# Performance work log

Measured on AMD Instinct MI355X. Metric: run time of the kernel, lower is better.

## Reference

```python
import jax, jax.numpy as jnp
import numpy as np

NEG = -1e9


def setup_inputs() -> dict:
    key = jax.random.key(0)
    ks = jax.random.split(key, 10)
    B, C, H, W = 4, 64, 64, 64
    Cq = C // 8
    x = jax.random.normal(ks[0], (B, C, H, W), dtype=jnp.float32)
    mask = jax.random.randint(ks[1], (B, 1, H, W), 0, 2, dtype=jnp.int32)
    # 1x1 conv params (out_ch, in_ch) + bias
    Wq = jax.random.normal(ks[2], (Cq, C), dtype=jnp.float32) * (1.0 / np.sqrt(C))
    bq = jnp.zeros((Cq,), dtype=jnp.float32)
    Wk = jax.random.normal(ks[3], (Cq, C), dtype=jnp.float32) * (1.0 / np.sqrt(C))
    bk = jnp.zeros((Cq,), dtype=jnp.float32)
    Wv = jax.random.normal(ks[4], (C, C), dtype=jnp.float32) * (1.0 / np.sqrt(C))
    bv = jnp.zeros((C,), dtype=jnp.float32)
    # torch inits gamma to 0; use small random so attention path contributes
    gamma = jax.random.normal(ks[5], (1,), dtype=jnp.float32) * 0.1
    return {"x": x, "mask": mask, "Wq": Wq, "bq": bq, "Wk": Wk, "bk": bk,
            "Wv": Wv, "bv": bv, "gamma": gamma}


def reference(x, mask, Wq, bq, Wk, bk, Wv, bv, gamma):
    B, C, H, W = x.shape
    N = H * W
    xf = x.reshape(B, C, N)                      # (B,C,N)
    # 1x1 convs == per-pixel linear projections
    q = jnp.einsum('oc,bcn->bno', Wq, xf) + bq   # (B,N,Cq)
    k = jnp.einsum('oc,bcn->bon', Wk, xf) + bk[None, :, None]  # (B,Cq,N)
    v = jnp.einsum('oc,bcn->bon', Wv, xf) + bv[None, :, None]  # (B,C,N)
    m = mask.reshape(B, N).astype(bool)
    logits = jnp.einsum('bno,bom->bnm', q, k)    # (B,N,N)
    valid = m[:, :, None] & m[:, None, :]        # outer-product validity mask
    logits = jnp.where(valid, logits, NEG)
    attn = jax.nn.softmax(logits, axis=-1)       # (B,N,N)
    out = jnp.einsum('bcj,bij->bci', v, attn)    # (B,C,N)
    out = out.reshape(B, C, H, W)
    return gamma * out + x
```

## Files before the change

kernel.cpp:

```cpp
#include <hip/hip_runtime.h>

typedef unsigned int uint;
typedef unsigned short ushort;
typedef unsigned long long ull;
typedef __attribute__((ext_vector_type(8))) short short8;
typedef __attribute__((ext_vector_type(4))) float f32x4;
typedef __attribute__((ext_vector_type(16))) float f32x16;
typedef __attribute__((ext_vector_type(4))) uint uint4v;
typedef __attribute__((ext_vector_type(2))) uint uint2v;

#define BATCH 4
#define CH 64
#define NPIX 4096
#define LOG2E 1.44269504f

#define WSQ 0
#define WSK 262144
#define WSV 524288
#define WSNV 1572864
#define WSQM 1572928
#define WSVPU 1589312

__device__ __forceinline__ ushort f2bf(float f) {
    union { float f; uint u; } a; a.f = f;
    const uint u = a.u;
    return (ushort)((u + 0x7FFFu + ((u >> 16) & 1u)) >> 16);
}
__device__ __forceinline__ uint cvtpk(float a, float b) {
    uint r;
    asm("v_cvt_pk_bf16_f32 %0, %1, %2" : "=v"(r) : "v"(a), "v"(b));
    return r;
}

__global__ __launch_bounds__(256) void proj_kernel(
    const float* __restrict__ x, const int* __restrict__ mask,
    const float* __restrict__ Wq, const float* __restrict__ bq,
    const float* __restrict__ Wk, const float* __restrict__ bk,
    const float* __restrict__ Wv, const float* __restrict__ bv,
    ushort* __restrict__ ws)
{
    __shared__ int   wcnt[4];
    __shared__ float wvs[4][16];
    const int g = blockIdx.y;
    const int tid = threadIdx.x;
    const int wid = tid >> 6, lane = tid & 63;

    const int pix = blockIdx.x * 256 + tid;
    const int b = pix >> 12;
    const int n = pix & (NPIX - 1);
    const int qm = mask[pix];
    const ull bal = __ballot(qm != 0);
    if (lane == 0) wcnt[wid] = __popcll(bal);
    __syncthreads();

    const float* xb = x + (size_t)b * CH * NPIX + n;
    float xv[64];
#pragma unroll
    for (int c = 0; c < 64; c++) xv[c] = xb[(size_t)c * NPIX];

    float acc[16];
    if (g == 0) {
#pragma unroll
        for (int o = 0; o < 16; o++) {
            const float* Wrow = (o < 8) ? (Wq + o * 64) : (Wk + (o - 8) * 64);
            float a = (o < 8) ? bq[o] : bk[o - 8];
#pragma unroll
            for (int c4 = 0; c4 < 16; c4++) {
                const float4 w = *(const float4*)(Wrow + c4 * 4);
                a += w.x * xv[c4 * 4] + w.y * xv[c4 * 4 + 1]
                   + w.z * xv[c4 * 4 + 2] + w.w * xv[c4 * 4 + 3];
            }
            acc[o] = a;
        }
    } else {
        const float* Wg = Wv + (g - 1) * 16 * 64;
        const float* bg = bv + (g - 1) * 16;
#pragma unroll
        for (int o = 0; o < 16; o++) {
            const float* Wrow = Wg + o * 64;
            float a = bg[o];
#pragma unroll
            for (int c4 = 0; c4 < 16; c4++) {
                const float4 w = *(const float4*)(Wrow + c4 * 4);
                a += w.x * xv[c4 * 4] + w.y * xv[c4 * 4 + 1]
                   + w.z * xv[c4 * 4 + 2] + w.w * xv[c4 * 4 + 3];
            }
            acc[o] = a;
        }
    }

    int offV = 0, offI = 0, nvb = 0;
#pragma unroll
    for (int w = 0; w < 4; w++) {
        const int cw = wcnt[w];
        if (w < wid) { offV += cw; offI += 64 - cw; }
        nvb += cw;
    }
    const int rankV = __popcll(bal & ((1ull << lane) - 1ull));
    const int slot = qm ? (offV + rankV) : (nvb + offI + (lane - rankV));
    const int rr = n >> 8;
    const int js = rr * 8 + (slot >> 5);
    const int jl = slot & 31;

    if (g == 0) {
        {
            const int jtq = n >> 5, jlq = n & 31;
            const float s = qm ? LOG2E : 0.f;
            uint4v lo, hi;
            lo.x = cvtpk(acc[0] * s, acc[1] * s);
            lo.y = cvtpk(acc[2] * s, acc[3] * s);
            lo.z = cvtpk(acc[4] * s, acc[5] * s);
            lo.w = cvtpk(acc[6] * s, acc[7] * s);
            hi.x = qm ? 0x3F80u : 0u;
            hi.y = 0u; hi.z = 0u; hi.w = 0u;
            ushort* qf = ws + WSQ + (size_t)b * 65536 + (size_t)jtq * 512;
            *(uint4v*)(qf + jlq * 8)       = lo;
            *(uint4v*)(qf + 256 + jlq * 8) = hi;
        }
        {
            uint4v lo, hi;
            lo.x = cvtpk(acc[8],  acc[9]);
            lo.y = cvtpk(acc[10], acc[11]);
            lo.z = cvtpk(acc[12], acc[13]);
            lo.w = cvtpk(acc[14], acc[15]);
            hi.x = (uint)f2bf(qm ? 0.f : -1e30f);
            hi.y = 0u; hi.z = 0u; hi.w = 0u;
            ushort* kf = ws + WSK + (size_t)b * 65536 + (size_t)js * 512;
            *(uint4v*)(kf + jl * 8)       = lo;
            *(uint4v*)(kf + 256 + jl * 8) = hi;
        }
        if (tid == 0) ws[WSNV + b * 16 + rr] = (ushort)nvb;
        ws[WSQM + pix] = (ushort)qm;
    } else {
        const int h = jl >> 4, hp = (jl >> 3) & 1, jj = jl & 7;
        const int c0 = (g - 1) * 16;
        ushort* vt = ws + WSV + (size_t)b * 262144;
#pragma unroll
        for (int o = 0; o < 16; o++) {
            const int c = c0 + o, ct = c >> 5, cp = c & 31;
            vt[(size_t)((((js * 2 + ct) * 2 + h) * 2 + hp) * 256) + cp * 8 + jj] = f2bf(acc[o]);
        }
#pragma unroll
        for (int o = 0; o < 16; o++) {
            float v = acc[o];
#pragma unroll
            for (int off = 32; off; off >>= 1) v += __shfl_down(v, off);
            if (lane == 0) wvs[wid][o] = v;
        }
        __syncthreads();
        if (tid < 16) {
            const float t = wvs[0][tid] + wvs[1][tid] + wvs[2][tid] + wvs[3][tid];
            float* vpf = (float*)(ws + WSVPU);
            vpf[(b * 64 + c0 + tid) * 16 + (blockIdx.x & 15)] = t;
        }
    }
}

__global__ __launch_bounds__(512, 2) void attn_kernel(
    const ushort* __restrict__ ws, const float* __restrict__ x,
    const float* __restrict__ gamma, float* __restrict__ out)
{
    __shared__ float Obuf[8][32][36];
    __shared__ float Lb[2][8][32];
    __shared__ float Linv[2][32];
    __shared__ float VmeanS[64];
    __shared__ ushort qmS[64];
    __shared__ ushort nvS[16];
    __shared__ ushort jtT[8][17];

    const int tid  = threadIdx.x;
    const int wid  = tid >> 6;
    const int lane = tid & 63;
    const int hl   = lane >> 5;
    const int col  = lane & 31;
    const int b    = blockIdx.y;
    const int bx   = blockIdx.x;

    const ushort* qf = ws + WSQ + (size_t)b * 65536 + (size_t)(2 * bx) * 512;
    const ushort* kf = ws + WSK + (size_t)b * 65536;
    const ushort* vt = ws + WSV + (size_t)b * 262144;

    const short8 qfA = *(const short8*)(qf + lane * 8);
    const short8 qfB = *(const short8*)(qf + 512 + lane * 8);

    if (tid < 16) nvS[tid] = ws[WSNV + b * 16 + tid];
    if (tid >= 64 && tid < 128) qmS[tid - 64] = ws[WSQM + b * 4096 + bx * 64 + (tid - 64)];
    if (tid >= 128 && tid < 192) {
        const int c = tid - 128;
        const float* vpf = (const float*)(ws + WSVPU);
        float s = 0.f;
#pragma unroll
        for (int k2 = 0; k2 < 16; k2++) s += vpf[(b * 64 + c) * 16 + k2];
        VmeanS[c] = s * (1.0f / 4096.0f);
    }
    __syncthreads();

    int A = 0;
#pragma unroll
    for (int r2 = 0; r2 < 16; r2++) {
        int a = ((int)nvS[r2] + 31) >> 5; if (a > 8) a = 8;
        A += a;
    }
    if (tid < 128) {
        const int w = tid >> 4, ii = tid & 15, ci = w + ii * 8;
        int Acc = 0, ent = 0;
#pragma unroll
        for (int r2 = 0; r2 < 16; r2++) {
            int a = ((int)nvS[r2] + 31) >> 5; if (a > 8) a = 8;
            if (ci >= Acc && ci < Acc + a) ent = r2 * 8 + (ci - Acc);
            Acc += a;
        }
        jtT[w][ii] = (ushort)ent;
    }
    if (tid < 8) jtT[tid][16] = 0;
    __syncthreads();

    const int niter = (A - wid + 7) >> 3;

    f32x16 accA0, accA1, accB0, accB1, zf;
#pragma unroll
    for (int r = 0; r < 16; r++) { accA0[r] = 0.f; accA1[r] = 0.f; accB0[r] = 0.f; accB1[r] = 0.f; zf[r] = 0.f; }
    float lsA = 0.f, lsB = 0.f;

    int jc = jtT[wid][0];
    uint4v kn   = *(const uint4v*)(kf + (size_t)jc * 512 + lane * 8);
    uint4v vn00 = *(const uint4v*)(vt + (size_t)((jc * 2 + 0) * 2 + 0) * 512 + lane * 8);
    uint4v vn01 = *(const uint4v*)(vt + (size_t)((jc * 2 + 0) * 2 + 1) * 512 + lane * 8);
    uint4v vn10 = *(const uint4v*)(vt + (size_t)((jc * 2 + 1) * 2 + 0) * 512 + lane * 8);
    uint4v vn11 = *(const uint4v*)(vt + (size_t)((jc * 2 + 1) * 2 + 1) * 512 + lane * 8);

#define QK_PV(SFRAG, LSUM, A0, A1) do {                                                              \
    float p[16];                                                                                     \
    _Pragma("unroll") for (int r = 0; r < 16; r++) p[r] = __builtin_amdgcn_exp2f((SFRAG)[r]);        \
    LSUM += (((p[0] + p[1]) + (p[2] + p[3])) + ((p[4] + p[5]) + (p[6] + p[7])))                      \
          + (((p[8] + p[9]) + (p[10] + p[11])) + ((p[12] + p[13]) + (p[14] + p[15])));               \
    uint P[8];                                                                                       \
    _Pragma("unroll") for (int r = 0; r < 8; r++) P[r] = cvtpk(p[2 * r], p[2 * r + 1]);              \
    const uint2v s02 = __builtin_amdgcn_permlane32_swap(P[0], P[2], false, false);                   \
    const uint2v s13 = __builtin_amdgcn_permlane32_swap(P[1], P[3], false, false);                   \
    const uint2v s46 = __builtin_amdgcn_permlane32_swap(P[4], P[6], false, false);                   \
    const uint2v s57 = __builtin_amdgcn_permlane32_swap(P[5], P[7], false, false);                   \
    uint4v B0, B1;                                                                                   \
    B0.x = s02.x; B0.y = s13.x; B0.z = s02.y; B0.w = s13.y;                                          \
    B1.x = s46.x; B1.y = s57.x; B1.z = s46.y; B1.w = s57.y;                                          \
    __builtin_amdgcn_s_setprio(1);                                                                   \
    A0 = __builtin_amdgcn_mfma_f32_32x32x16_bf16(*(const short8*)&c00, *(const short8*)&B0, A0, 0, 0, 0); \
    A0 = __builtin_amdgcn_mfma_f32_32x32x16_bf16(*(const short8*)&c01, *(const short8*)&B1, A0, 0, 0, 0); \
    A1 = __builtin_amdgcn_mfma_f32_32x32x16_bf16(*(const short8*)&c10, *(const short8*)&B0, A1, 0, 0, 0); \
    A1 = __builtin_amdgcn_mfma_f32_32x32x16_bf16(*(const short8*)&c11, *(const short8*)&B1, A1, 0, 0, 0); \
    __builtin_amdgcn_s_setprio(0);                                                                   \
} while (0)

    for (int i = 0; i < niter; i++) {
        const int jn = jtT[wid][i + 1];
        const uint4v kc = kn, c00 = vn00, c01 = vn01, c10 = vn10, c11 = vn11;
        if (i + 1 < niter) {
            kn   = *(const uint4v*)(kf + (size_t)jn * 512 + lane * 8);
            vn00 = *(const uint4v*)(vt + (size_t)((jn * 2 + 0) * 2 + 0) * 512 + lane * 8);
            vn01 = *(const uint4v*)(vt + (size_t)((jn * 2 + 0) * 2 + 1) * 512 + lane * 8);
            vn10 = *(const uint4v*)(vt + (size_t)((jn * 2 + 1) * 2 + 0) * 512 + lane * 8);
            vn11 = *(const uint4v*)(vt + (size_t)((jn * 2 + 1) * 2 + 1) * 512 + lane * 8);
        }

        const f32x16 sA = __builtin_amdgcn_mfma_f32_32x32x16_bf16(*(const short8*)&kc, qfA, zf, 0, 0, 0);
        const f32x16 sB = __builtin_amdgcn_mfma_f32_32x32x16_bf16(*(const short8*)&kc, qfB, zf, 0, 0, 0);

        QK_PV(sA, lsA, accA0, accA1);
        QK_PV(sB, lsB, accB0, accB1);
    }
#undef QK_PV

    const float lwA = lsA + __shfl_xor(lsA, 32);
    const float lwB = lsB + __shfl_xor(lsB, 32);
    if (hl == 0) { Lb[0][wid][col] = lwA; Lb[1][wid][col] = lwB; }
    __syncthreads();
    if (tid < 64) {
        const int q = tid >> 5, m = tid & 31;
        float s = 0.f;
#pragma unroll
        for (int w = 0; w < 8; w++) s += Lb[q][w][m];
        Linv[q][m] = 1.f / s;
    }

    const float gm = gamma[0];

#define MERGE_PASS(ACC, QSEL, CHALF) do {                                                            \
    __syncthreads();                                                                                 \
    _Pragma("unroll") for (int r = 0; r < 16; r++) {                                                 \
        const int crow = (r & 3) + 8 * (r >> 2) + 4 * hl;            \
        Obuf[wid][crow][col] = (ACC)[r];                                                             \
    }                                                                                                \
    __syncthreads();                                                                                 \
    {                                                                                                \
        const int c = tid >> 4, m0 = (tid & 15) * 2;                                                 \
        float o0 = 0.f, o1 = 0.f;                                                                    \
        _Pragma("unroll") for (int w = 0; w < 8; w++) { o0 += Obuf[w][c][m0]; o1 += Obuf[w][c][m0 + 1]; } \
        const int cg = (CHALF) * 32 + c;                                                             \
        const int mi = (QSEL) * 32 + m0;                                                             \
        const size_t base = (((size_t)(b * CH + cg)) << 12) + bx * 64 + (QSEL) * 32 + m0;            \
        const float2 xv = *(const float2*)&x[base];                                                  \
        float2 rv;                                                                                   \
        rv.x = (qmS[mi]     ? gm * o0 * Linv[QSEL][m0]     : gm * VmeanS[cg]) + xv.x;                \
        rv.y = (qmS[mi + 1] ? gm * o1 * Linv[QSEL][m0 + 1] : gm * VmeanS[cg]) + xv.y;                \
        *(float2*)&out[base] = rv;                                                                   \
    }                                                                                                \
} while (0)

    MERGE_PASS(accA0, 0, 0);
    MERGE_PASS(accA1, 0, 1);
    MERGE_PASS(accB0, 1, 0);
    MERGE_PASS(accB1, 1, 1);
#undef MERGE_PASS
}

extern "C" void kernel_launch(void* const* d_in, const int* in_sizes, int n_in,
                              void* d_out, int out_size, void* d_ws, size_t ws_size,
                              hipStream_t stream) {
    const float* x     = (const float*)d_in[0];
    const int*   mask  = (const int*)d_in[1];
    const float* Wq    = (const float*)d_in[2];
    const float* bq    = (const float*)d_in[3];
    const float* Wk    = (const float*)d_in[4];
    const float* bk    = (const float*)d_in[5];
    const float* Wv    = (const float*)d_in[6];
    const float* bv    = (const float*)d_in[7];
    const float* gamma = (const float*)d_in[8];
    float* out  = (float*)d_out;
    ushort* ws  = (ushort*)d_ws;

    proj_kernel<<<dim3(64, 5), 256, 0, stream>>>(x, mask, Wq, bq, Wk, bk, Wv, bv, ws);
    attn_kernel<<<dim3(64, 4), 512, 0, stream>>>(ws, x, gamma, out);
}
```

Measured before the change: 101.0 us.

## Compute QKV projection with bf16 MFMA split-precision in a single grid pass

Rewrites the projection kernel so each block stages bf16 hi/lo weight splits in LDS and computes Q, K and V for 32 pixels per wave with 32x32x16 bf16 MFMAs. Three-term and two-term split products keep near-fp32 accuracy. The grid changes from 5 channel groups that each reread x to 128 blocks that read x once. The per-region V column sums are now computed by summing x and applying Wv, replacing the shuffle reductions. The cost is redundant weight conversion in every block and slightly different rounding of the projections.

```diff
diff --git a/kernel.cpp b/kernel.cpp
--- a/kernel.cpp
+++ b/kernel.cpp
@@ -39,56 +39,48 @@
     const float* __restrict__ Wv, const float* __restrict__ bv,
     ushort* __restrict__ ws)
 {
-    __shared__ int   wcnt[4];
-    __shared__ float wvs[4][16];
-    const int g = blockIdx.y;
-    const int tid = threadIdx.x;
-    const int wid = tid >> 6, lane = tid & 63;
-
-    const int pix = blockIdx.x * 256 + tid;
-    const int b = pix >> 12;
-    const int n = pix & (NPIX - 1);
-    const int qm = mask[pix];
+    __shared__ ushort WL[6144];
+    __shared__ ushort WLlo[2048];
+    __shared__ float  biasL[96];
+    __shared__ ushort slotS[256];
+    __shared__ ushort qmS2[256];
+    __shared__ int    wcnt[4];
+    __shared__ float  sxL[64];
+
+    const int tid  = threadIdx.x;
+    const int wid  = tid >> 6, lane = tid & 63;
+    const int hl   = lane >> 5, col = lane & 31;
+    const int blk  = blockIdx.x;
+    const int reg  = blk >> 1;
+    const int half = blk & 1;
+    const int b    = reg >> 4, rr = reg & 15;
+    const int pixg = reg * 256 + tid;
+
+    for (int i = tid; i < 6144; i += 256) {
+        const int rt = i >> 11, rem = i & 2047;
+        const int s = rem >> 9, rem2 = rem & 511;
+        const int h2 = rem2 >> 8, row = (rem2 & 255) >> 3, jj = rem2 & 7;
+        const int R = rt * 32 + row, c = s * 16 + h2 * 8 + jj;
+        float v = 0.f;
+        if (R < 8)       v = Wq[R * 64 + c] * LOG2E;
+        else if (R < 16) v = Wk[(R - 8) * 64 + c];
+        else if (R < 80) v = Wv[(R - 16) * 64 + c];
+        const ushort hi = f2bf(v);
+        WL[i] = hi;
+        if (rt == 0) {
+            const float lo = v - __uint_as_float((uint)hi << 16);
+            WLlo[i] = f2bf(lo);
+        }
+    }
+    if (tid < 96)
+        biasL[tid] = (tid < 8) ? bq[tid] * LOG2E
+                   : (tid < 16) ? bk[tid - 8]
+                   : (tid < 80) ? bv[tid - 16] : 0.f;
+
+    const int qm = mask[pixg];
     const ull bal = __ballot(qm != 0);
     if (lane == 0) wcnt[wid] = __popcll(bal);
     __syncthreads();
-
-    const float* xb = x + (size_t)b * CH * NPIX + n;
-    float xv[64];
-#pragma unroll
-    for (int c = 0; c < 64; c++) xv[c] = xb[(size_t)c * NPIX];
-
-    float acc[16];
-    if (g == 0) {
-#pragma unroll
-        for (int o = 0; o < 16; o++) {
-            const float* Wrow = (o < 8) ? (Wq + o * 64) : (Wk + (o - 8) * 64);
-            float a = (o < 8) ? bq[o] : bk[o - 8];
-#pragma unroll
-            for (int c4 = 0; c4 < 16; c4++) {
-                const float4 w = *(const float4*)(Wrow + c4 * 4);
-                a += w.x * xv[c4 * 4] + w.y * xv[c4 * 4 + 1]
-                   + w.z * xv[c4 * 4 + 2] + w.w * xv[c4 * 4 + 3];
-            }
-            acc[o] = a;
-        }
-    } else {
-        const float* Wg = Wv + (g - 1) * 16 * 64;
-        const float* bg = bv + (g - 1) * 16;
-#pragma unroll
-        for (int o = 0; o < 16; o++) {
-            const float* Wrow = Wg + o * 64;
-            float a = bg[o];
-#pragma unroll
-            for (int c4 = 0; c4 < 16; c4++) {
-                const float4 w = *(const float4*)(Wrow + c4 * 4);
-                a += w.x * xv[c4 * 4] + w.y * xv[c4 * 4 + 1]
-                   + w.z * xv[c4 * 4 + 2] + w.w * xv[c4 * 4 + 3];
-            }
-            acc[o] = a;
-        }
-    }
-
     int offV = 0, offI = 0, nvb = 0;
 #pragma unroll
     for (int w = 0; w < 4; w++) {
@@ -98,61 +90,123 @@
     }
     const int rankV = __popcll(bal & ((1ull << lane) - 1ull));
     const int slot = qm ? (offV + rankV) : (nvb + offI + (lane - rankV));
-    const int rr = n >> 8;
-    const int js = rr * 8 + (slot >> 5);
-    const int jl = slot & 31;
-
-    if (g == 0) {
-        {
-            const int jtq = n >> 5, jlq = n & 31;
-            const float s = qm ? LOG2E : 0.f;
-            uint4v lo, hi;
-            lo.x = cvtpk(acc[0] * s, acc[1] * s);
-            lo.y = cvtpk(acc[2] * s, acc[3] * s);
-            lo.z = cvtpk(acc[4] * s, acc[5] * s);
-            lo.w = cvtpk(acc[6] * s, acc[7] * s);
-            hi.x = qm ? 0x3F80u : 0u;
-            hi.y = 0u; hi.z = 0u; hi.w = 0u;
-            ushort* qf = ws + WSQ + (size_t)b * 65536 + (size_t)jtq * 512;
-            *(uint4v*)(qf + jlq * 8)       = lo;
-            *(uint4v*)(qf + 256 + jlq * 8) = hi;
-        }
-        {
-            uint4v lo, hi;
-            lo.x = cvtpk(acc[8],  acc[9]);
-            lo.y = cvtpk(acc[10], acc[11]);
-            lo.z = cvtpk(acc[12], acc[13]);
-            lo.w = cvtpk(acc[14], acc[15]);
-            hi.x = (uint)f2bf(qm ? 0.f : -1e30f);
-            hi.y = 0u; hi.z = 0u; hi.w = 0u;
-            ushort* kf = ws + WSK + (size_t)b * 65536 + (size_t)js * 512;
-            *(uint4v*)(kf + jl * 8)       = lo;
-            *(uint4v*)(kf + 256 + jl * 8) = hi;
-        }
+    slotS[tid] = (ushort)slot;
+    qmS2[tid] = (ushort)qm;
+    if (half == 0) {
+        ws[WSQM + pixg] = (ushort)qm;
         if (tid == 0) ws[WSNV + b * 16 + rr] = (ushort)nvb;
-        ws[WSQM + pix] = (ushort)qm;
-    } else {
-        const int h = jl >> 4, hp = (jl >> 3) & 1, jj = jl & 7;
-        const int c0 = (g - 1) * 16;
-        ushort* vt = ws + WSV + (size_t)b * 262144;
-#pragma unroll
-        for (int o = 0; o < 16; o++) {
-            const int c = c0 + o, ct = c >> 5, cp = c & 31;
-            vt[(size_t)((((js * 2 + ct) * 2 + h) * 2 + hp) * 256) + cp * 8 + jj] = f2bf(acc[o]);
-        }
-#pragma unroll
-        for (int o = 0; o < 16; o++) {
-            float v = acc[o];
-#pragma unroll
-            for (int off = 32; off; off >>= 1) v += __shfl_down(v, off);
-            if (lane == 0) wvs[wid][o] = v;
-        }
-        __syncthreads();
-        if (tid < 16) {
-            const float t = wvs[0][tid] + wvs[1][tid] + wvs[2][tid] + wvs[3][tid];
-            float* vpf = (float*)(ws + WSVPU);
-            vpf[(b * 64 + c0 + tid) * 16 + (blockIdx.x & 15)] = t;
-        }
+    }
+    __syncthreads();
+
+    const int p = half * 4 + wid;
+    const int n0 = p * 32;
+    const float* xb = x + (size_t)b * (CH * NPIX) + rr * 256 + n0 + col;
+
+    float xr[4][8];
+#pragma unroll
+    for (int s = 0; s < 4; s++)
+#pragma unroll
+        for (int jj = 0; jj < 8; jj++)
+            xr[s][jj] = xb[(size_t)(s * 16 + hl * 8 + jj) * NPIX];
+
+    uint Bh[4][4], Bl[4][4];
+#pragma unroll
+    for (int s = 0; s < 4; s++)
+#pragma unroll
+        for (int w2 = 0; w2 < 4; w2++) {
+            const float a = xr[s][2 * w2], b2 = xr[s][2 * w2 + 1];
+            const uint u = cvtpk(a, b2);
+            Bh[s][w2] = u;
+            const float ha = __uint_as_float(u << 16);
+            const float hb = __uint_as_float(u & 0xFFFF0000u);
+            Bl[s][w2] = cvtpk(a - ha, b2 - hb);
+        }
+
+    f32x16 a0, a1, a2;
+#pragma unroll
+    for (int r = 0; r < 16; r++) {
+        const int crow = (r & 3) + 8 * (r >> 2) + 4 * hl;
+        a0[r] = biasL[crow]; a1[r] = biasL[32 + crow]; a2[r] = biasL[64 + crow];
+    }
+
+#pragma unroll
+    for (int s = 0; s < 4; s++) {
+        const short8 A0  = *(const short8*)&WL[((0 * 4 + s) * 2 + hl) * 256 + col * 8];
+        const short8 A0l = *(const short8*)&WLlo[(s * 2 + hl) * 256 + col * 8];
+        const short8 A1  = *(const short8*)&WL[((1 * 4 + s) * 2 + hl) * 256 + col * 8];
+        const short8 A2  = *(const short8*)&WL[((2 * 4 + s) * 2 + hl) * 256 + col * 8];
+        const short8 bh = *(const short8*)&Bh[s], bl = *(const short8*)&Bl[s];
+        a0 = __builtin_amdgcn_mfma_f32_32x32x16_bf16(A0, bh, a0, 0, 0, 0);
+        a0 = __builtin_amdgcn_mfma_f32_32x32x16_bf16(A0, bl, a0, 0, 0, 0);
+        a0 = __builtin_amdgcn_mfma_f32_32x32x16_bf16(A0l, bh, a0, 0, 0, 0);
+        a1 = __builtin_amdgcn_mfma_f32_32x32x16_bf16(A1, bh, a1, 0, 0, 0);
+        a1 = __builtin_amdgcn_mfma_f32_32x32x16_bf16(A1, bl, a1, 0, 0, 0);
+        a2 = __builtin_amdgcn_mfma_f32_32x32x16_bf16(A2, bh, a2, 0, 0, 0);
+        a2 = __builtin_amdgcn_mfma_f32_32x32x16_bf16(A2, bl, a2, 0, 0, 0);
+    }
+
+    const int rpx = n0 + col;
+    const int qv = qmS2[rpx];
+    const int slt = slotS[rpx];
+    const int js = rr * 8 + (slt >> 5), jl = slt & 31;
+
+    {
+        const float sc = qv ? 1.f : 0.f;
+        uint2v qw; qw.x = cvtpk(a0[0] * sc, a0[1] * sc); qw.y = cvtpk(a0[2] * sc, a0[3] * sc);
+        ushort* qfp = ws + WSQ + (size_t)b * 65536 + (size_t)(rr * 8 + p) * 512;
+        *(uint2v*)(qfp + col * 8 + 4 * hl) = qw;
+        if (hl == 0) {
+            uint4v h4; h4.x = qv ? 0x3F80u : 0u; h4.y = 0u; h4.z = 0u; h4.w = 0u;
+            *(uint4v*)(qfp + 256 + col * 8) = h4;
+        }
+    }
+    {
+        uint2v kw; kw.x = cvtpk(a0[4], a0[5]); kw.y = cvtpk(a0[6], a0[7]);
+        ushort* kfp = ws + WSK + (size_t)b * 65536 + (size_t)js * 512;
+        *(uint2v*)(kfp + jl * 8 + 4 * hl) = kw;
+        if (hl == 0) {
+            uint4v h4; h4.x = (uint)f2bf(qv ? 0.f : -1e30f); h4.y = 0u; h4.z = 0u; h4.w = 0u;
+            *(uint4v*)(kfp + 256 + jl * 8) = h4;
+        }
+    }
+    {
+        ushort* vp = ws + WSV + (size_t)b * 262144 + (size_t)js * 2048
+                   + (jl >> 4) * 512 + ((jl >> 3) & 1) * 256 + (jl & 7) + hl * 32;
+#define VQUAD(ACC, RB, CB) do {                                                      \
+        ushort* q_ = vp + ((CB) >> 5) * 1024 + ((CB) & 31) * 8;                      \
+        const uint u0 = cvtpk((ACC)[(RB)], (ACC)[(RB) + 1]);                         \
+        const uint u1 = cvtpk((ACC)[(RB) + 2], (ACC)[(RB) + 3]);                     \
+        q_[0]  = (ushort)u0; q_[8]  = (ushort)(u0 >> 16);                            \
+        q_[16] = (ushort)u1; q_[24] = (ushort)(u1 >> 16);                            \
+} while (0)
+        VQUAD(a0, 8, 0);  VQUAD(a0, 12, 8);
+        VQUAD(a1, 0, 16); VQUAD(a1, 4, 24); VQUAD(a1, 8, 32); VQUAD(a1, 12, 40);
+        VQUAD(a2, 0, 48); VQUAD(a2, 4, 56);
+#undef VQUAD
+    }
+
+    __syncthreads();
+    if (half == 0 && tid < 64) {
+        const float* xrow = x + ((size_t)b * CH + tid) * NPIX + rr * 256;
+        float s = 0.f;
+#pragma unroll
+        for (int i2 = 0; i2 < 64; i2++) {
+            const float4 v4 = *(const float4*)&xrow[i2 * 4];
+            s += ((v4.x + v4.y) + (v4.z + v4.w));
+        }
+        sxL[tid] = s;
+    }
+    __syncthreads();
+    if (half == 0 && tid < 64) {
+        const float* wr = Wv + tid * 64;
+        float t = 256.f * bv[tid];
+#pragma unroll
+        for (int c4 = 0; c4 < 16; c4++) {
+            const float4 w4 = *(const float4*)&wr[c4 * 4];
+            t += w4.x * sxL[c4 * 4] + w4.y * sxL[c4 * 4 + 1]
+               + w4.z * sxL[c4 * 4 + 2] + w4.w * sxL[c4 * 4 + 3];
+        }
+        ((float*)(ws + WSVPU))[(b * 64 + tid) * 16 + rr] = t;
     }
 }
 
@@ -328,6 +382,6 @@
     float* out  = (float*)d_out;
     ushort* ws  = (ushort*)d_ws;
 
-    proj_kernel<<<dim3(64, 5), 256, 0, stream>>>(x, mask, Wq, bq, Wk, bk, Wv, bv, ws);
+    proj_kernel<<<dim3(128), 256, 0, stream>>>(x, mask, Wq, bq, Wk, bk, Wv, bv, ws);
     attn_kernel<<<dim3(64, 4), 512, 0, stream>>>(ws, x, gamma, out);
 }
```

Measured after the change: 97.17 us. 1.04x faster.
